# Performance work log

Hardware: AMD Instinct MI355X
Metric: run time of the kernel (lower is better)

## Reference

```python
import jax, jax.numpy as jnp
import numpy as np

B, S, D = 2, 2048, 1024
H, DK, DV = 16, 64, 64
N_WINDOW = 256
LN_EPS = 1e-5


def setup_inputs() -> dict:
    key = jax.random.key(0)
    ks = jax.random.split(key, 8)
    sc = 0.02
    return {
        "Q": jax.random.normal(ks[0], (B, S, D), jnp.float32),
        "K": jax.random.normal(ks[1], (B, S, D), jnp.float32),
        "V": jax.random.normal(ks[2], (B, S, D), jnp.float32),
        "Wq": jax.random.normal(ks[3], (D, H * DK), jnp.float32) * sc,
        "bq": jnp.zeros((H * DK,), jnp.float32),
        "Wk": jax.random.normal(ks[4], (D, H * DK), jnp.float32) * sc,
        "bk": jnp.zeros((H * DK,), jnp.float32),
        "Wv": jax.random.normal(ks[5], (D, H * DV), jnp.float32) * sc,
        "bv": jnp.zeros((H * DV,), jnp.float32),
        "Wo": jax.random.normal(ks[6], (H * DV, D), jnp.float32) * sc,
        "bo": jnp.zeros((D,), jnp.float32),
        "gamma": jnp.ones((D,), jnp.float32),
        "beta": jnp.zeros((D,), jnp.float32),
    }


def reference(Q, K, V, Wq, bq, Wk, bk, Wv, bv, Wo, bo, gamma, beta):
    b, s, _ = Q.shape
    # QKV projections -> [b, s, h, d]
    q = (Q @ Wq + bq).reshape(b, s, H, DK)
    k = (K @ Wk + bk).reshape(b, s, H, DK)
    v = (V @ Wv + bv).reshape(b, s, H, DV)
    # scores [b, h, i, j]
    scores = jnp.einsum("bihd,bjhd->bhij", q, k) / np.sqrt(DK).astype(np.float32)
    # sliding-window band mask |i - j| < N_WINDOW (mask=True path)
    idx = jnp.arange(s)
    band = jnp.abs(idx[:, None] - idx[None, :]) < N_WINDOW  # [s, s]
    scores = jnp.where(band[None, None], scores, -jnp.inf)
    attn = jax.nn.softmax(scores, axis=-1)
    ctx = jnp.einsum("bhij,bjhd->bihd", attn, v).reshape(b, s, H * DV)
    out = ctx @ Wo + bo
    # residual + LayerNorm over last dim
    x = out + Q
    mu = jnp.mean(x, axis=-1, keepdims=True)
    var = jnp.mean(jnp.square(x - mu), axis=-1, keepdims=True)
    y = (x - mu) * jax.lax.rsqrt(var + LN_EPS) * gamma + beta
    return y, attn
```

## Files before the change

### kernel.cpp

```cpp
#include <hip/hip_runtime.h>
#include <hip/hip_bf16.h>

#define BB 2
#define SS 2048
#define HH 16
#define LN_EPS 1e-5f
#define LOG2E 1.44269504088896f

typedef __attribute__((ext_vector_type(8))) short short8;
typedef __attribute__((ext_vector_type(4))) float floatx4;

#define EXP2F(x) __builtin_amdgcn_exp2f(x)
#define GLOAD16(g, l) __builtin_amdgcn_global_load_lds( \
    (const __attribute__((address_space(1))) void*)(g), \
    (__attribute__((address_space(3))) void*)(l), 16, 0, 0)

__device__ __forceinline__ ushort f2b(float f) {
    union { float f; unsigned u; } x; x.f = f;
    unsigned u = x.u;
    return (ushort)((u + 0x7FFFu + ((u >> 16) & 1u)) >> 16);
}
__device__ __forceinline__ float b2f(ushort u) {
    union { unsigned u; float f; } x; x.u = ((unsigned)u) << 16;
    return x.f;
}

__global__ __launch_bounds__(256) void to_bf16(
    const float* __restrict__ X0, const float* __restrict__ X1, const float* __restrict__ X2,
    ushort* __restrict__ Y0, ushort* __restrict__ Y1, ushort* __restrict__ Y2)
{
    const int z = blockIdx.z;
    const float* X = z == 0 ? X0 : z == 1 ? X1 : X2;
    ushort* Y = z == 0 ? Y0 : z == 1 ? Y1 : Y2;
    const size_t i = ((size_t)blockIdx.x * 256 + threadIdx.x) * 8;
    float4 a = *(const float4*)&X[i];
    float4 b = *(const float4*)&X[i + 4];
    short8 o;
    o[0] = (short)f2b(a.x); o[1] = (short)f2b(a.y); o[2] = (short)f2b(a.z); o[3] = (short)f2b(a.w);
    o[4] = (short)f2b(b.x); o[5] = (short)f2b(b.y); o[6] = (short)f2b(b.z); o[7] = (short)f2b(b.w);
    *(short8*)&Y[i] = o;
}

__global__ __launch_bounds__(256) void wtrans(
    const float* __restrict__ W0, const float* __restrict__ W1,
    const float* __restrict__ W2, const float* __restrict__ W3,
    ushort* __restrict__ T0, ushort* __restrict__ T1,
    ushort* __restrict__ T2, ushort* __restrict__ T3)
{
    const int z = blockIdx.z;
    const float* W = z == 0 ? W0 : z == 1 ? W1 : z == 2 ? W2 : W3;
    ushort* T = z == 0 ? T0 : z == 1 ? T1 : z == 2 ? T2 : T3;
    const float scale = (z == 0) ? 0.125f : 1.0f;
    __shared__ float ts[32][33];
    const int k0 = blockIdx.y * 32, n0 = blockIdx.x * 32;
    const int r = threadIdx.x >> 3, c4 = (threadIdx.x & 7) * 4;
    float4 v = *(const float4*)&W[(size_t)(k0 + r) * 1024 + n0 + c4];
    ts[r][c4 + 0] = v.x; ts[r][c4 + 1] = v.y; ts[r][c4 + 2] = v.z; ts[r][c4 + 3] = v.w;
    __syncthreads();
    ushort4 o;
    o.x = f2b(ts[c4 + 0][r] * scale); o.y = f2b(ts[c4 + 1][r] * scale);
    o.z = f2b(ts[c4 + 2][r] * scale); o.w = f2b(ts[c4 + 3][r] * scale);
    *(ushort4*)&T[(size_t)(n0 + r) * 1024 + k0 + c4] = o;
}

__device__ __forceinline__ void gemm_body(
    const ushort* __restrict__ Ab, const ushort* __restrict__ Bt,
    const float* __restrict__ bias, float bscale,
    float* Cf, ushort* Cb, int m0, int n0)
{
    __shared__ ushort As[128 * 32];
    __shared__ ushort Bs[128 * 32];
    const int t = threadIdx.x;
    const int l = t & 63;
    const int w = t >> 6;
    const int wm = w >> 1, wn = w & 1;

    floatx4 acc[4][4] = {};

    const int i0c = w * 64 + l;
    const int r0 = i0c >> 2, c0 = i0c & 3;
    const int i1c = 256 + i0c;
    const int r1 = i1c >> 2, c1 = i1c & 3;

    const ushort* gA0 = &Ab[(size_t)(m0 + r0) * 1024 + c0 * 8];
    const ushort* gA1 = &Ab[(size_t)(m0 + r1) * 1024 + c1 * 8];
    const ushort* gB0 = &Bt[(size_t)(n0 + r0) * 1024 + c0 * 8];
    const ushort* gB1 = &Bt[(size_t)(n0 + r1) * 1024 + c1 * 8];

    char* lA = (char*)As;
    char* lB = (char*)Bs;
    const int d0 = (w * 64) * 16;
    const int d1 = (256 + w * 64) * 16;

    for (int k0 = 0; k0 < 1024; k0 += 32) {
        __syncthreads();
        GLOAD16(gA0 + k0, lA + d0);
        GLOAD16(gA1 + k0, lA + d1);
        GLOAD16(gB0 + k0, lB + d0);
        GLOAD16(gB1 + k0, lB + d1);
        __syncthreads();

        short8 af[4], bf[4];
#pragma unroll
        for (int m = 0; m < 4; ++m)
            af[m] = *(const short8*)&As[(wm * 64 + m * 16 + (l & 15)) * 32 + (l >> 4) * 8];
#pragma unroll
        for (int n = 0; n < 4; ++n)
            bf[n] = *(const short8*)&Bs[(wn * 64 + n * 16 + (l & 15)) * 32 + (l >> 4) * 8];
#pragma unroll
        for (int m = 0; m < 4; ++m)
#pragma unroll
            for (int n = 0; n < 4; ++n)
                acc[m][n] = __builtin_amdgcn_mfma_f32_16x16x32_bf16(af[m], bf[n], acc[m][n], 0, 0, 0);
    }

    const int cr = (l >> 4) * 4;
    const int cc = l & 15;
#pragma unroll
    for (int n = 0; n < 4; ++n) {
        int col = n0 + wn * 64 + n * 16 + cc;
        float bv = bias[col] * bscale;
#pragma unroll
        for (int m = 0; m < 4; ++m) {
            int row = m0 + wm * 64 + m * 16 + cr;
#pragma unroll
            for (int j = 0; j < 4; ++j) {
                float v = acc[m][n][j] + bv;
                if (Cf) Cf[(size_t)(row + j) * 1024 + col] = v;
                else    Cb[(size_t)(row + j) * 1024 + col] = f2b(v);
            }
        }
    }
}

__device__ __forceinline__ void swz_mn(int& m0, int& n0) {
    int bid = blockIdx.x + (blockIdx.y << 3);
    int xcd = bid & 7, idx = bid >> 3;
    m0 = (xcd * 4 + (idx & 3)) * 128;
    n0 = (idx >> 2) * 128;
}

__global__ __launch_bounds__(256) void gemm_qkv(
    const ushort* __restrict__ Xq, const ushort* __restrict__ Xk, const ushort* __restrict__ Xv,
    const ushort* __restrict__ Wqt, const ushort* __restrict__ Wkt, const ushort* __restrict__ Wvt,
    const float* __restrict__ bq, const float* __restrict__ bk, const float* __restrict__ bv,
    ushort* __restrict__ qp, ushort* __restrict__ kp, ushort* __restrict__ vp)
{
    const int z = blockIdx.z;
    const ushort* A = z == 0 ? Xq : z == 1 ? Xk : Xv;
    const ushort* Bt = z == 0 ? Wqt : z == 1 ? Wkt : Wvt;
    const float* bias = z == 0 ? bq : z == 1 ? bk : bv;
    ushort* C = z == 0 ? qp : z == 1 ? kp : vp;
    float bscale = (z == 0) ? 0.125f : 1.0f;
    int m0, n0; swz_mn(m0, n0);
    gemm_body(A, Bt, bias, bscale, nullptr, C, m0, n0);
}

__global__ __launch_bounds__(256) void gemm_obf(
    const ushort* __restrict__ ctxb, const ushort* __restrict__ Wot,
    const float* __restrict__ bo, float* __restrict__ op)
{
    int m0, n0; swz_mn(m0, n0);
    gemm_body(ctxb, Wot, bo, 1.0f, op, nullptr, m0, n0);
}

__global__ __launch_bounds__(256, 4) void attn_mfma(
    const ushort* __restrict__ qb, const ushort* __restrict__ kb, const ushort* __restrict__ vb,
    float* __restrict__ attn, ushort* __restrict__ ctxb)
{
    __shared__ alignas(16) ushort Ks[64 * 72];
    __shared__ alignas(16) ushort Vt[64 * 72];
    __shared__ alignas(16) ushort Pl[4][16 * 72];

    const int qblk = blockIdx.x, h = blockIdx.y, b = blockIdx.z;
    const int i0 = qblk * 64;
    const int t = threadIdx.x;
    const int w = t >> 6, l = t & 63;
    const int g = l >> 4, c = l & 15;
    const int ibase = i0 + w * 16;

    const int jstart = max(0, i0 - 256);
    const int jend = min(SS, i0 + 64 + 256);

    const size_t qoff = (size_t)(b * SS + ibase + c) * 1024 + h * 64 + g * 8;
    short8 aq0 = *(const short8*)&qb[qoff];
    short8 aq1 = *(const short8*)&qb[qoff + 32];

    const int krow = t >> 2, kd0 = (t & 3) * 16;
    const int vj0 = (t & 31) * 2, vd0 = (t >> 5) * 8;

    float m[4] = {-3e38f, -3e38f, -3e38f, -3e38f};
    float ll[4] = {0.f, 0.f, 0.f, 0.f};

    for (int jt = jstart; jt < jend; jt += 64) {
        __syncthreads();
        {
            const ushort* kr = &kb[(size_t)(b * SS + jt + krow) * 1024 + h * 64 + kd0];
            short8 k0 = *(const short8*)kr;
            short8 k1 = *(const short8*)(kr + 8);
            *(short8*)&Ks[krow * 72 + kd0] = k0;
            *(short8*)&Ks[krow * 72 + kd0 + 8] = k1;
        }
        __syncthreads();
        floatx4 s[4] = {};
#pragma unroll
        for (int u = 0; u < 4; ++u) {
            short8 b0 = *(const short8*)&Ks[(u * 16 + c) * 72 + g * 8];
            short8 b1 = *(const short8*)&Ks[(u * 16 + c) * 72 + 32 + g * 8];
            s[u] = __builtin_amdgcn_mfma_f32_16x16x32_bf16(aq0, b0, s[u], 0, 0, 0);
            s[u] = __builtin_amdgcn_mfma_f32_16x16x32_bf16(aq1, b1, s[u], 0, 0, 0);
        }
        const bool full = (jt >= ibase - 240) && (jt <= ibase + 192);
#pragma unroll
        for (int r = 0; r < 4; ++r) {
            float v0 = s[0][r] * LOG2E, v1 = s[1][r] * LOG2E,
                  v2 = s[2][r] * LOG2E, v3 = s[3][r] * LOG2E;
            if (!full) {
                const int i = ibase + g * 4 + r;
                const int j0 = jt + c;
                if ((unsigned)(i - j0 + 255) >= 511u)        v0 = -3e38f;
                if ((unsigned)(i - (j0 + 16) + 255) >= 511u) v1 = -3e38f;
                if ((unsigned)(i - (j0 + 32) + 255) >= 511u) v2 = -3e38f;
                if ((unsigned)(i - (j0 + 48) + 255) >= 511u) v3 = -3e38f;
            }
            float tmax = fmaxf(fmaxf(v0, v1), fmaxf(v2, v3));
            float mn = fmaxf(m[r], tmax);
            float sc_ = EXP2F(m[r] - mn);
            float add = EXP2F(v0 - mn) + EXP2F(v1 - mn)
                      + EXP2F(v2 - mn) + EXP2F(v3 - mn);
            ll[r] = ll[r] * sc_ + add;
            m[r] = mn;
        }
    }

    float M[4], invL[4];
#pragma unroll
    for (int r = 0; r < 4; ++r) {
        float mm = m[r];
        mm = fmaxf(mm, __shfl_xor(mm, 1));
        mm = fmaxf(mm, __shfl_xor(mm, 2));
        mm = fmaxf(mm, __shfl_xor(mm, 4));
        mm = fmaxf(mm, __shfl_xor(mm, 8));
        float la = ll[r] * EXP2F(m[r] - mm);
        la += __shfl_xor(la, 1);
        la += __shfl_xor(la, 2);
        la += __shfl_xor(la, 4);
        la += __shfl_xor(la, 8);
        M[r] = mm;
        invL[r] = 1.0f / la;
    }

    floatx4 ctx[4] = {};
    for (int jt = jstart; jt < jend; jt += 64) {
        __syncthreads();
        {
            const ushort* kr = &kb[(size_t)(b * SS + jt + krow) * 1024 + h * 64 + kd0];
            short8 k0 = *(const short8*)kr;
            short8 k1 = *(const short8*)(kr + 8);
            *(short8*)&Ks[krow * 72 + kd0] = k0;
            *(short8*)&Ks[krow * 72 + kd0 + 8] = k1;
        }
        {
            const ushort* vr = &vb[(size_t)(b * SS + jt + vj0) * 1024 + h * 64 + vd0];
            short8 v0 = *(const short8*)vr;
            short8 v1 = *(const short8*)(vr + 1024);
#pragma unroll
            for (int e = 0; e < 8; ++e) {
                ushort2 pr;
                pr.x = (ushort)v0[e];
                pr.y = (ushort)v1[e];
                *(ushort2*)&Vt[(vd0 + e) * 72 + vj0] = pr;
            }
        }
        __syncthreads();
        floatx4 s[4] = {};
#pragma unroll
        for (int u = 0; u < 4; ++u) {
            short8 b0 = *(const short8*)&Ks[(u * 16 + c) * 72 + g * 8];
            short8 b1 = *(const short8*)&Ks[(u * 16 + c) * 72 + 32 + g * 8];
            s[u] = __builtin_amdgcn_mfma_f32_16x16x32_bf16(aq0, b0, s[u], 0, 0, 0);
            s[u] = __builtin_amdgcn_mfma_f32_16x16x32_bf16(aq1, b1, s[u], 0, 0, 0);
        }
        const bool full = (jt >= ibase - 240) && (jt <= ibase + 192);
#pragma unroll
        for (int u = 0; u < 4; ++u) {
#pragma unroll
            for (int r = 0; r < 4; ++r) {
                float v = s[u][r] * LOG2E;
                if (!full) {
                    const int i = ibase + g * 4 + r;
                    const int j = jt + u * 16 + c;
                    if ((unsigned)(i - j + 255) >= 511u) v = -3e38f;
                }
                float p = EXP2F(v - M[r]) * invL[r];
                Pl[w][(g * 4 + r) * 72 + u * 16 + c] = f2b(p);
            }
        }
#pragma unroll
        for (int it = 0; it < 4; ++it) {
            const int row = it * 4 + g;
            ushort4 pw = *(const ushort4*)&Pl[w][row * 72 + c * 4];
            floatx4 o;
            o[0] = b2f(pw.x); o[1] = b2f(pw.y); o[2] = b2f(pw.z); o[3] = b2f(pw.w);
            __builtin_nontemporal_store(o,
                (floatx4*)&attn[(size_t)(b * HH + h) * SS * SS + (size_t)(ibase + row) * SS + jt + c * 4]);
        }
#pragma unroll
        for (int jc = 0; jc < 2; ++jc) {
            short8 pa = *(const short8*)&Pl[w][c * 72 + jc * 32 + g * 8];
#pragma unroll
            for (int ds = 0; ds < 4; ++ds) {
                short8 bv_ = *(const short8*)&Vt[(ds * 16 + c) * 72 + jc * 32 + g * 8];
                ctx[ds] = __builtin_amdgcn_mfma_f32_16x16x32_bf16(pa, bv_, ctx[ds], 0, 0, 0);
            }
        }
    }

#pragma unroll
    for (int ds = 0; ds < 4; ++ds)
#pragma unroll
        for (int r = 0; r < 4; ++r)
            ctxb[(size_t)(b * SS + ibase + g * 4 + r) * 1024 + h * 64 + ds * 16 + c] = f2b(ctx[ds][r]);

    {
        float* ab = attn + (size_t)(b * HH + h) * SS * SS;
        const floatx4 z4 = {0.f, 0.f, 0.f, 0.f};
        const int g16 = t >> 4, c16 = t & 15;
#pragma unroll
        for (int rr = 0; rr < 4; ++rr) {
            float* rp = ab + (size_t)(i0 + g16 + rr * 16) * SS;
            for (int x = c16 * 4; x < jstart; x += 64)
                __builtin_nontemporal_store(z4, (floatx4*)&rp[x]);
            for (int x = jend + c16 * 4; x < SS; x += 64)
                __builtin_nontemporal_store(z4, (floatx4*)&rp[x]);
        }
    }
}

__global__ __launch_bounds__(256) void ln_kernel(
    const float* __restrict__ op, const float* __restrict__ Qin,
    const float* __restrict__ gamma, const float* __restrict__ beta,
    float* __restrict__ y)
{
    const int row = blockIdx.x;
    const int t = threadIdx.x;
    __shared__ float rs[4], rss[4];

    float4 o4 = *(const float4*)&op[(size_t)row * 1024 + t * 4];
    float4 q4 = *(const float4*)&Qin[(size_t)row * 1024 + t * 4];
    float x0 = o4.x + q4.x, x1 = o4.y + q4.y, x2 = o4.z + q4.z, x3 = o4.w + q4.w;
    float s = x0 + x1 + x2 + x3;
    float ss = x0 * x0 + x1 * x1 + x2 * x2 + x3 * x3;
#pragma unroll
    for (int off = 1; off < 64; off <<= 1) {
        s  += __shfl_xor(s, off, 64);
        ss += __shfl_xor(ss, off, 64);
    }
    int wid = t >> 6;
    if ((t & 63) == 0) { rs[wid] = s; rss[wid] = ss; }
    __syncthreads();
    s  = rs[0] + rs[1] + rs[2] + rs[3];
    ss = rss[0] + rss[1] + rss[2] + rss[3];
    float mu = s * (1.0f / 1024.0f);
    float var = ss * (1.0f / 1024.0f) - mu * mu;
    float rstd = rsqrtf(var + LN_EPS);
    float4 g4 = *(const float4*)&gamma[t * 4];
    float4 b4 = *(const float4*)&beta[t * 4];
    float4 o;
    o.x = (x0 - mu) * rstd * g4.x + b4.x;
    o.y = (x1 - mu) * rstd * g4.y + b4.y;
    o.z = (x2 - mu) * rstd * g4.z + b4.z;
    o.w = (x3 - mu) * rstd * g4.w + b4.w;
    *(float4*)&y[(size_t)row * 1024 + t * 4] = o;
}

extern "C" void kernel_launch(void* const* d_in, const int* in_sizes, int n_in,
                              void* d_out, int out_size, void* d_ws, size_t ws_size,
                              hipStream_t stream) {
    (void)in_sizes; (void)n_in; (void)out_size; (void)ws_size;
    const float* Q  = (const float*)d_in[0];
    const float* K  = (const float*)d_in[1];
    const float* V  = (const float*)d_in[2];
    const float* Wq = (const float*)d_in[3];
    const float* bq = (const float*)d_in[4];
    const float* Wk = (const float*)d_in[5];
    const float* bk = (const float*)d_in[6];
    const float* Wv = (const float*)d_in[7];
    const float* bv = (const float*)d_in[8];
    const float* Wo = (const float*)d_in[9];
    const float* bo = (const float*)d_in[10];
    const float* gamma = (const float*)d_in[11];
    const float* beta  = (const float*)d_in[12];

    float* y = (float*)d_out;
    float* attn = y + (size_t)BB * SS * 1024;

    char* base = (char*)d_ws;
    float*  op   = (float*)base;
    ushort* Xq   = (ushort*)base;
    ushort* Xk   = (ushort*)(base + (size_t)8 * 1048576);
    ushort* Xv   = (ushort*)(base + (size_t)16 * 1048576);
    ushort* ctxb = (ushort*)(base + (size_t)16 * 1048576);
    ushort* qbp  = (ushort*)(base + (size_t)24 * 1048576);
    ushort* kbp  = (ushort*)(base + (size_t)32 * 1048576);
    ushort* vbp  = (ushort*)(base + (size_t)40 * 1048576);
    ushort* Wqt  = (ushort*)(base + (size_t)48 * 1048576);
    ushort* Wkt  = (ushort*)(base + (size_t)50 * 1048576);
    ushort* Wvt  = (ushort*)(base + (size_t)52 * 1048576);
    ushort* Wot  = (ushort*)(base + (size_t)54 * 1048576);

    to_bf16<<<dim3(2048, 1, 3), 256, 0, stream>>>(Q, K, V, Xq, Xk, Xv);
    wtrans<<<dim3(32, 32, 4), 256, 0, stream>>>(Wq, Wk, Wv, Wo, Wqt, Wkt, Wvt, Wot);
    gemm_qkv<<<dim3(8, 32, 3), 256, 0, stream>>>(Xq, Xk, Xv, Wqt, Wkt, Wvt, bq, bk, bv, qbp, kbp, vbp);
    attn_mfma<<<dim3(SS / 64, HH, BB), 256, 0, stream>>>(qbp, kbp, vbp, attn, ctxb);
    gemm_obf<<<dim3(8, 32), 256, 0, stream>>>(ctxb, Wot, bo, op);
    ln_kernel<<<4096, 256, 0, stream>>>(op, Q, gamma, beta, y);
}
```

Measured before the change: 232.0 us.

## Double-buffer GEMM and V tiles; read K fragments directly from global

The projection GEMM now double-buffers its LDS A/B tiles. The next k-slice is issued via global_load_lds before computing on the current one, and each iteration needs one barrier instead of two. In the attention kernel, K fragments are loaded straight from global memory into MFMA operands, which removes the K staging to LDS and its barriers. V is double-buffered, with the next tile prefetched into registers and transposed into the alternate buffer after the PV MFMAs. This trades LDS traffic and synchronization for more uncoalesced global/L2 reads of K and extra LDS and register footprint. The GEMM prefetch may race, since global_load_lds completion is not waited on before the loop-end barrier without an explicit vmcnt wait.

```diff
diff --git a/kernel.cpp b/kernel.cpp
--- a/kernel.cpp
+++ b/kernel.cpp
@@ -68,8 +68,8 @@
     const float* __restrict__ bias, float bscale,
     float* Cf, ushort* Cb, int m0, int n0)
 {
-    __shared__ ushort As[128 * 32];
-    __shared__ ushort Bs[128 * 32];
+    __shared__ ushort As[2][128 * 32];
+    __shared__ ushort Bs[2][128 * 32];
     const int t = threadIdx.x;
     const int l = t & 63;
     const int w = t >> 6;
@@ -87,31 +87,37 @@
     const ushort* gB0 = &Bt[(size_t)(n0 + r0) * 1024 + c0 * 8];
     const ushort* gB1 = &Bt[(size_t)(n0 + r1) * 1024 + c1 * 8];
 
-    char* lA = (char*)As;
-    char* lB = (char*)Bs;
     const int d0 = (w * 64) * 16;
     const int d1 = (256 + w * 64) * 16;
 
+    GLOAD16(gA0, (char*)As[0] + d0);
+    GLOAD16(gA1, (char*)As[0] + d1);
+    GLOAD16(gB0, (char*)Bs[0] + d0);
+    GLOAD16(gB1, (char*)Bs[0] + d1);
+    __syncthreads();
+
+    int cur = 0;
     for (int k0 = 0; k0 < 1024; k0 += 32) {
-        __syncthreads();
-        GLOAD16(gA0 + k0, lA + d0);
-        GLOAD16(gA1 + k0, lA + d1);
-        GLOAD16(gB0 + k0, lB + d0);
-        GLOAD16(gB1 + k0, lB + d1);
-        __syncthreads();
-
+        if (k0 + 32 < 1024) {
+            GLOAD16(gA0 + k0 + 32, (char*)As[cur ^ 1] + d0);
+            GLOAD16(gA1 + k0 + 32, (char*)As[cur ^ 1] + d1);
+            GLOAD16(gB0 + k0 + 32, (char*)Bs[cur ^ 1] + d0);
+            GLOAD16(gB1 + k0 + 32, (char*)Bs[cur ^ 1] + d1);
+        }
         short8 af[4], bf[4];
 #pragma unroll
         for (int m = 0; m < 4; ++m)
-            af[m] = *(const short8*)&As[(wm * 64 + m * 16 + (l & 15)) * 32 + (l >> 4) * 8];
+            af[m] = *(const short8*)&As[cur][(wm * 64 + m * 16 + (l & 15)) * 32 + (l >> 4) * 8];
 #pragma unroll
         for (int n = 0; n < 4; ++n)
-            bf[n] = *(const short8*)&Bs[(wn * 64 + n * 16 + (l & 15)) * 32 + (l >> 4) * 8];
+            bf[n] = *(const short8*)&Bs[cur][(wn * 64 + n * 16 + (l & 15)) * 32 + (l >> 4) * 8];
 #pragma unroll
         for (int m = 0; m < 4; ++m)
 #pragma unroll
             for (int n = 0; n < 4; ++n)
                 acc[m][n] = __builtin_amdgcn_mfma_f32_16x16x32_bf16(af[m], bf[n], acc[m][n], 0, 0, 0);
+        __syncthreads();
+        cur ^= 1;
     }
 
     const int cr = (l >> 4) * 4;
@@ -168,8 +174,7 @@
     const ushort* __restrict__ qb, const ushort* __restrict__ kb, const ushort* __restrict__ vb,
     float* __restrict__ attn, ushort* __restrict__ ctxb)
 {
-    __shared__ alignas(16) ushort Ks[64 * 72];
-    __shared__ alignas(16) ushort Vt[64 * 72];
+    __shared__ alignas(16) ushort Vt[2][64 * 72];
     __shared__ alignas(16) ushort Pl[4][16 * 72];
 
     const int qblk = blockIdx.x, h = blockIdx.y, b = blockIdx.z;
@@ -186,27 +191,19 @@
     short8 aq0 = *(const short8*)&qb[qoff];
     short8 aq1 = *(const short8*)&qb[qoff + 32];
 
-    const int krow = t >> 2, kd0 = (t & 3) * 16;
     const int vj0 = (t & 31) * 2, vd0 = (t >> 5) * 8;
+    const ushort* Kbh = &kb[(size_t)(b * SS) * 1024 + h * 64];
 
     float m[4] = {-3e38f, -3e38f, -3e38f, -3e38f};
     float ll[4] = {0.f, 0.f, 0.f, 0.f};
 
     for (int jt = jstart; jt < jend; jt += 64) {
-        __syncthreads();
-        {
-            const ushort* kr = &kb[(size_t)(b * SS + jt + krow) * 1024 + h * 64 + kd0];
-            short8 k0 = *(const short8*)kr;
-            short8 k1 = *(const short8*)(kr + 8);
-            *(short8*)&Ks[krow * 72 + kd0] = k0;
-            *(short8*)&Ks[krow * 72 + kd0 + 8] = k1;
-        }
-        __syncthreads();
+        const ushort* kt = Kbh + (size_t)jt * 1024;
         floatx4 s[4] = {};
 #pragma unroll
         for (int u = 0; u < 4; ++u) {
-            short8 b0 = *(const short8*)&Ks[(u * 16 + c) * 72 + g * 8];
-            short8 b1 = *(const short8*)&Ks[(u * 16 + c) * 72 + 32 + g * 8];
+            short8 b0 = *(const short8*)&kt[(size_t)(u * 16 + c) * 1024 + g * 8];
+            short8 b1 = *(const short8*)&kt[(size_t)(u * 16 + c) * 1024 + 32 + g * 8];
             s[u] = __builtin_amdgcn_mfma_f32_16x16x32_bf16(aq0, b0, s[u], 0, 0, 0);
             s[u] = __builtin_amdgcn_mfma_f32_16x16x32_bf16(aq1, b1, s[u], 0, 0, 0);
         }
@@ -250,34 +247,34 @@
         invL[r] = 1.0f / la;
     }
 
+    {
+        const ushort* vr = &vb[(size_t)(b * SS + jstart + vj0) * 1024 + h * 64 + vd0];
+        short8 v0 = *(const short8*)vr;
+        short8 v1 = *(const short8*)(vr + 1024);
+#pragma unroll
+        for (int e = 0; e < 8; ++e) {
+            ushort2 pr; pr.x = (ushort)v0[e]; pr.y = (ushort)v1[e];
+            *(ushort2*)&Vt[0][(vd0 + e) * 72 + vj0] = pr;
+        }
+    }
+    __syncthreads();
+
     floatx4 ctx[4] = {};
+    int cur = 0;
     for (int jt = jstart; jt < jend; jt += 64) {
-        __syncthreads();
-        {
-            const ushort* kr = &kb[(size_t)(b * SS + jt + krow) * 1024 + h * 64 + kd0];
-            short8 k0 = *(const short8*)kr;
-            short8 k1 = *(const short8*)(kr + 8);
-            *(short8*)&Ks[krow * 72 + kd0] = k0;
-            *(short8*)&Ks[krow * 72 + kd0 + 8] = k1;
-        }
-        {
-            const ushort* vr = &vb[(size_t)(b * SS + jt + vj0) * 1024 + h * 64 + vd0];
-            short8 v0 = *(const short8*)vr;
-            short8 v1 = *(const short8*)(vr + 1024);
-#pragma unroll
-            for (int e = 0; e < 8; ++e) {
-                ushort2 pr;
-                pr.x = (ushort)v0[e];
-                pr.y = (ushort)v1[e];
-                *(ushort2*)&Vt[(vd0 + e) * 72 + vj0] = pr;
-            }
-        }
-        __syncthreads();
+        const bool have = (jt + 64 < jend);
+        short8 nv0, nv1;
+        if (have) {
+            const ushort* vr = &vb[(size_t)(b * SS + jt + 64 + vj0) * 1024 + h * 64 + vd0];
+            nv0 = *(const short8*)vr;
+            nv1 = *(const short8*)(vr + 1024);
+        }
+        const ushort* kt = Kbh + (size_t)jt * 1024;
         floatx4 s[4] = {};
 #pragma unroll
         for (int u = 0; u < 4; ++u) {
-            short8 b0 = *(const short8*)&Ks[(u * 16 + c) * 72 + g * 8];
-            short8 b1 = *(const short8*)&Ks[(u * 16 + c) * 72 + 32 + g * 8];
+            short8 b0 = *(const short8*)&kt[(size_t)(u * 16 + c) * 1024 + g * 8];
+            short8 b1 = *(const short8*)&kt[(size_t)(u * 16 + c) * 1024 + 32 + g * 8];
             s[u] = __builtin_amdgcn_mfma_f32_16x16x32_bf16(aq0, b0, s[u], 0, 0, 0);
             s[u] = __builtin_amdgcn_mfma_f32_16x16x32_bf16(aq1, b1, s[u], 0, 0, 0);
         }
@@ -310,10 +307,19 @@
             short8 pa = *(const short8*)&Pl[w][c * 72 + jc * 32 + g * 8];
 #pragma unroll
             for (int ds = 0; ds < 4; ++ds) {
-                short8 bv_ = *(const short8*)&Vt[(ds * 16 + c) * 72 + jc * 32 + g * 8];
+                short8 bv_ = *(const short8*)&Vt[cur][(ds * 16 + c) * 72 + jc * 32 + g * 8];
                 ctx[ds] = __builtin_amdgcn_mfma_f32_16x16x32_bf16(pa, bv_, ctx[ds], 0, 0, 0);
             }
         }
+        if (have) {
+#pragma unroll
+            for (int e = 0; e < 8; ++e) {
+                ushort2 pr; pr.x = (ushort)nv0[e]; pr.y = (ushort)nv1[e];
+                *(ushort2*)&Vt[cur ^ 1][(vd0 + e) * 72 + vj0] = pr;
+            }
+        }
+        __syncthreads();
+        cur ^= 1;
     }
 
 #pragma unroll
```

Result: no change. 236.6 us (+2.0%).
